# Optimization experiments

Hardware: AMD Instinct MI355X
Metric: run time of the kernel (lower is better)

Reference implementation:

```python
import jax, jax.numpy as jnp
import numpy as np

B, S, D, H = 4, 2048, 1024, 16
HD = D // H
NEG = -1e30


def setup_inputs() -> dict:
    key = jax.random.key(0)
    ks = jax.random.split(key, 6)
    scale = 1.0 / np.sqrt(D)
    return {
        "q": jax.random.normal(ks[0], (B, S, D), jnp.float32),
        "k": jax.random.normal(ks[1], (B, S, D), jnp.float32),
        "v": jax.random.normal(ks[2], (B, S, D), jnp.float32),
        "mask": jnp.ones((B, 1, S), jnp.float32),
        "wq": jax.random.normal(ks[3], (D, D), jnp.float32) * scale,
        "bq": jnp.zeros((D,), jnp.float32),
        "wk": jax.random.normal(ks[4], (D, D), jnp.float32) * scale,
        "bk": jnp.zeros((D,), jnp.float32),
        "wv": jax.random.normal(ks[5], (D, D), jnp.float32) * scale,
        "bv": jnp.zeros((D,), jnp.float32),
    }


def _heads(x):
    # (B,S,D) -> (B,H,S,HD)
    return x.reshape(B, S, H, HD).transpose(0, 2, 1, 3)


def reference(q, k, v, mask, wq, bq, wk, bk, wv, bv):
    # pointwise Conv1D(kernel=1) == linear: x @ W^T + b (W: (out,in))
    qh = _heads(jnp.einsum('bsd,ed->bse', q, wq) + bq)
    kh = _heads(jnp.einsum('bsd,ed->bse', k, wk) + bk)
    vh = _heads(jnp.einsum('bsd,ed->bse', v, wv) + bv)
    scores = jnp.einsum('bhqd,bhkd->bhqk', qh, kh) / jnp.sqrt(jnp.float32(HD))
    # mask_logits: x + (1 - mask) * -1e30, mask (B,1,S) -> (B,1,1,S)
    scores = scores + (1.0 - mask[:, None, :, :]) * NEG
    probs = jax.nn.softmax(scores, axis=-1)  # dropout is identity in eval
    ctx = jnp.einsum('bhqk,bhkd->bhqd', probs, vh)
    return ctx.transpose(0, 2, 1, 3).reshape(B, S, D)
```

## Files before the change

### kernel.cpp

```cpp
#include <hip/hip_runtime.h>
#include <math.h>

typedef __attribute__((ext_vector_type(8)))  _Float16 f16x8;
typedef __attribute__((ext_vector_type(4)))  _Float16 f16x4;
typedef __attribute__((ext_vector_type(2)))  __fp16   h16x2;
typedef __attribute__((ext_vector_type(4)))  float    f32x4;
typedef __attribute__((ext_vector_type(16))) float    f32x16;
typedef unsigned int u32;

static constexpr int B  = 4;
static constexpr int S  = 2048;
static constexpr int D  = 1024;
static constexpr int H  = 16;
static constexpr int HD = 64;

union U64cvt { f16x4 h; ushort4 u; };
union W4 { u32 w[4]; f16x8 v; };

__device__ __forceinline__ void gld16(const void* g, void* l) {
    __builtin_amdgcn_global_load_lds((const u32*)g, (u32*)l, 16, 0, 0);
}

__device__ __forceinline__ void cvtwr16(const float4& x, const float4& y, void* dst) {
    W4 w;
    w.w[0] = __builtin_bit_cast(u32, __builtin_amdgcn_cvt_pkrtz(x.x, x.y));
    w.w[1] = __builtin_bit_cast(u32, __builtin_amdgcn_cvt_pkrtz(x.z, x.w));
    w.w[2] = __builtin_bit_cast(u32, __builtin_amdgcn_cvt_pkrtz(y.x, y.y));
    w.w[3] = __builtin_bit_cast(u32, __builtin_amdgcn_cvt_pkrtz(y.z, y.w));
    *(f16x8*)dst = w.v;
}

__global__ __launch_bounds__(256)
void cvt_prep(const float* __restrict__ q, const float* __restrict__ k,
              const float* __restrict__ v,
              const float* __restrict__ wq, const float* __restrict__ wk,
              const float* __restrict__ wv,
              unsigned short* __restrict__ dst)
{
    const int c = blockIdx.x * 256 + threadIdx.x;
    const float* src;
    size_t idx;
    if (c < 3145728) {
        const int a = c >> 20;
        src = (a == 0) ? q : (a == 1) ? k : v;
        idx = (size_t)(c & 1048575) * 8;
    } else {
        const int c2 = c - 3145728;
        const int a = c2 >> 17;
        src = (a == 0) ? wq : (a == 1) ? wk : wv;
        idx = (size_t)(c2 & 131071) * 8;
    }
    const float4 x = *(const float4*)(src + idx);
    const float4 y = *(const float4*)(src + idx + 4);
    cvtwr16(x, y, dst + (size_t)c * 8);
}

__global__ __launch_bounds__(256)
void proj_f16(const unsigned short* __restrict__ af16,
              const unsigned short* __restrict__ wf16,
              const float* __restrict__ bqp, const float* __restrict__ bkp,
              const float* __restrict__ bvp,
              unsigned short* __restrict__ outs)
{
    const int bid = blockIdx.x;
    const int xcd = bid & 7;
    const int idx = bid >> 3;
    const int z   = idx / 64;
    const int r2  = idx - z * 64;
    const int mpl = r2 >> 3;
    const int np  = r2 & 7;
    const int mp  = (xcd >> 1) * 16 + (xcd & 1) * 8 + mpl;
    const int m0  = mp * 128;
    const int n0  = np * 128;

    const unsigned short* A  = af16 + (size_t)z * 8388608;
    const unsigned short* Wf = wf16 + (size_t)z * 1048576;
    const float* bias = (z == 0) ? bqp : (z == 1) ? bkp : bvp;
    unsigned short* out = outs + (size_t)z * 8388608;

    const int tid  = threadIdx.x;
    const int lane = tid & 63;
    const int wid  = tid >> 6;
    const int wr   = wid >> 1;
    const int wc   = wid & 1;

    __shared__ __align__(16) unsigned char lA[2][8192];
    __shared__ __align__(16) unsigned char lB[2][8192];

    f32x4 acc[4][4];
#pragma unroll
    for (int i = 0; i < 4; ++i)
#pragma unroll
        for (int j = 0; j < 4; ++j) acc[i][j] = (f32x4){0.f, 0.f, 0.f, 0.f};

    int grow[2], gcol[2], lbase[2];
#pragma unroll
    for (int i = 0; i < 2; ++i) {
        const int c = tid + 256 * i;
        grow[i]  = c >> 2;
        gcol[i]  = ((c & 3) - (grow[i] >> 1)) & 3;
        lbase[i] = (c & ~63) * 16;
    }

#pragma unroll
    for (int i = 0; i < 2; ++i) {
        gld16(A  + (size_t)(m0 + grow[i]) * D + gcol[i] * 8, lA[0] + lbase[i]);
        gld16(Wf + (size_t)(n0 + grow[i]) * D + gcol[i] * 8, lB[0] + lbase[i]);
    }
    __syncthreads();

    for (int kt = 0; kt < 32; ++kt) {
        const int cb = kt & 1, nx = cb ^ 1;

        if (kt < 31) {
            const int k1 = (kt + 1) * 32;
#pragma unroll
            for (int i = 0; i < 2; ++i) {
                gld16(A  + (size_t)(m0 + grow[i]) * D + k1 + gcol[i] * 8, lA[nx] + lbase[i]);
                gld16(Wf + (size_t)(n0 + grow[i]) * D + k1 + gcol[i] * 8, lB[nx] + lbase[i]);
            }
        }

        f16x8 af[4], bf[4];
#pragma unroll
        for (int mi = 0; mi < 4; ++mi) {
            const int row = wr * 64 + mi * 16 + (lane & 15);
            const int cc  = ((lane >> 4) + (row >> 1)) & 3;
            af[mi] = *(const f16x8*)(lA[cb] + row * 64 + cc * 16);
        }
#pragma unroll
        for (int ni = 0; ni < 4; ++ni) {
            const int row = wc * 64 + ni * 16 + (lane & 15);
            const int cc  = ((lane >> 4) + (row >> 1)) & 3;
            bf[ni] = *(const f16x8*)(lB[cb] + row * 64 + cc * 16);
        }

        __builtin_amdgcn_s_setprio(1);
#pragma unroll
        for (int mi = 0; mi < 4; ++mi)
#pragma unroll
            for (int ni = 0; ni < 4; ++ni)
                acc[mi][ni] = __builtin_amdgcn_mfma_f32_16x16x32_f16(af[mi], bf[ni], acc[mi][ni], 0, 0, 0);
        __builtin_amdgcn_s_setprio(0);

        __syncthreads();
    }

#pragma unroll
    for (int mi = 0; mi < 4; ++mi) {
        const int gmBase = m0 + wr * 64 + mi * 16 + ((lane >> 4) << 2);
        const int b  = gmBase >> 11;
        const int s0 = gmBase & 2047;
        const int tV   = s0 >> 6;
        const int kv6  = s0 & 63;
        const int ksg  = kv6 >> 4;
        const int hi2v = (kv6 >> 3) & 1;
        const int jb   = kv6 & 7;
#pragma unroll
        for (int ni = 0; ni < 4; ++ni) {
            const int gn = n0 + wc * 64 + ni * 16 + (lane & 15);
            const float bb = bias[gn];
            const int hh = gn >> 6;
            const int hd = gn & 63;
            const size_t bhbase = ((size_t)b * H + hh) * ((size_t)S * HD);
            if (z == 0) {
#pragma unroll
                for (int r = 0; r < 4; ++r) {
                    const int gm = gmBase + r;
                    const _Float16 hv = (_Float16)(acc[mi][ni][r] + bb);
                    out[bhbase + (size_t)(gm & 2047) * HD + hd] =
                        __builtin_bit_cast(unsigned short, hv);
                }
            } else if (z == 1) {
                const int ks   = hd >> 4;
                const int hi2k = (hd >> 3) & 1;
                const int j    = hd & 7;
#pragma unroll
                for (int r = 0; r < 4; ++r) {
                    const int s = (gmBase + r) & 2047;
                    const int t = s >> 6;
                    const int q = ((s >> 5) & 1) * 4 + ks;
                    const _Float16 hv = (_Float16)(acc[mi][ni][r] + bb);
                    out[bhbase + (((size_t)t * 8 + q) * 64 + hi2k * 32 + (s & 31)) * 8 + j] =
                        __builtin_bit_cast(unsigned short, hv);
                }
            } else {
                const int nb  = hd >> 5;
                const int c31 = hd & 31;
                const int q   = nb * 4 + ksg;
                U64cvt uu;
#pragma unroll
                for (int r = 0; r < 4; ++r)
                    uu.h[r] = (_Float16)(acc[mi][ni][r] + bb);
                *(ushort4*)(out + bhbase +
                    (((size_t)tV * 8 + q) * 64 + hi2v * 32 + c31) * 8 + jb) = uu.u;
            }
        }
    }
}

__global__ __launch_bounds__(256)
void proj_qkv(const float* __restrict__ qi, const float* __restrict__ ki,
              const float* __restrict__ vi,
              const float* __restrict__ wqp, const float* __restrict__ wkp,
              const float* __restrict__ wvp,
              const float* __restrict__ bqp, const float* __restrict__ bkp,
              const float* __restrict__ bvp,
              unsigned short* __restrict__ ws)
{
    const int bid = blockIdx.x;
    const int xcd = bid & 7;
    const int idx = bid >> 3;
    const int z   = idx / 64;
    const int r2  = idx - z * 64;
    const int mpl = r2 >> 3;
    const int np  = r2 & 7;
    const int mp  = (xcd >> 1) * 16 + (xcd & 1) * 8 + mpl;
    const int m0  = mp * 128;
    const int n0  = np * 128;

    const float* A    = (z == 0) ? qi  : (z == 1) ? ki  : vi;
    const float* W    = (z == 0) ? wqp : (z == 1) ? wkp : wvp;
    const float* bias = (z == 0) ? bqp : (z == 1) ? bkp : bvp;
    unsigned short* out = ws + (size_t)z * ((size_t)B * S * D);

    const int tid  = threadIdx.x;
    const int lane = tid & 63;
    const int wid  = tid >> 6;
    const int wr   = wid >> 1;
    const int wc   = wid & 1;

    __shared__ __align__(16) unsigned char lA[2][8192];
    __shared__ __align__(16) unsigned char lB[2][8192];

    f32x4 acc[4][4];
#pragma unroll
    for (int i = 0; i < 4; ++i)
#pragma unroll
        for (int j = 0; j < 4; ++j) acc[i][j] = (f32x4){0.f, 0.f, 0.f, 0.f};

    const int rb = (lane >> 4) * 16;

    int srow[2], sc8[2], soff[2];
#pragma unroll
    for (int i = 0; i < 2; ++i) {
        const int f = tid + 256 * i;
        srow[i] = f >> 2;
        sc8[i]  = f & 3;
        soff[i] = ((f >> 2) * 64 + (f & 3) * 16) ^ ((((f >> 2)) & 7) << 4);
    }

#pragma unroll
    for (int i = 0; i < 2; ++i) {
        const float* pa = A + (size_t)(m0 + srow[i]) * D + sc8[i] * 8;
        const float* pw = W + (size_t)(n0 + srow[i]) * D + sc8[i] * 8;
        cvtwr16(*(const float4*)pa, *(const float4*)(pa + 4), lA[0] + soff[i]);
        cvtwr16(*(const float4*)pw, *(const float4*)(pw + 4), lB[0] + soff[i]);
    }
    float4 pa0[2], pa1[2], pw0[2], pw1[2];
#pragma unroll
    for (int i = 0; i < 2; ++i) {
        const float* pa = A + (size_t)(m0 + srow[i]) * D + 32 + sc8[i] * 8;
        const float* pw = W + (size_t)(n0 + srow[i]) * D + 32 + sc8[i] * 8;
        pa0[i] = *(const float4*)pa;  pa1[i] = *(const float4*)(pa + 4);
        pw0[i] = *(const float4*)pw;  pw1[i] = *(const float4*)(pw + 4);
    }
    __syncthreads();

    for (int kt = 0; kt < 32; ++kt) {
        const int cb = kt & 1, nx = cb ^ 1;
        if (kt < 31) {
#pragma unroll
            for (int i = 0; i < 2; ++i) {
                cvtwr16(pa0[i], pa1[i], lA[nx] + soff[i]);
                cvtwr16(pw0[i], pw1[i], lB[nx] + soff[i]);
            }
        }
        f16x8 af[4], bf[4];
#pragma unroll
        for (int mi = 0; mi < 4; ++mi) {
            const int row = wr * 64 + mi * 16 + (lane & 15);
            af[mi] = *(const f16x8*)(lA[cb] + ((row * 64 + rb) ^ ((row & 7) << 4)));
        }
#pragma unroll
        for (int ni = 0; ni < 4; ++ni) {
            const int row = wc * 64 + ni * 16 + (lane & 15);
            bf[ni] = *(const f16x8*)(lB[cb] + ((row * 64 + rb) ^ ((row & 7) << 4)));
        }
        if (kt < 30) {
            const int k2 = (kt + 2) * 32;
#pragma unroll
            for (int i = 0; i < 2; ++i) {
                const float* pa = A + (size_t)(m0 + srow[i]) * D + k2 + sc8[i] * 8;
                const float* pw = W + (size_t)(n0 + srow[i]) * D + k2 + sc8[i] * 8;
                pa0[i] = *(const float4*)pa;  pa1[i] = *(const float4*)(pa + 4);
                pw0[i] = *(const float4*)pw;  pw1[i] = *(const float4*)(pw + 4);
            }
        }
        __builtin_amdgcn_s_setprio(1);
#pragma unroll
        for (int mi = 0; mi < 4; ++mi)
#pragma unroll
            for (int ni = 0; ni < 4; ++ni)
                acc[mi][ni] = __builtin_amdgcn_mfma_f32_16x16x32_f16(af[mi], bf[ni], acc[mi][ni], 0, 0, 0);
        __builtin_amdgcn_s_setprio(0);
        __syncthreads();
    }

#pragma unroll
    for (int mi = 0; mi < 4; ++mi) {
        const int gmBase = m0 + wr * 64 + mi * 16 + ((lane >> 4) << 2);
        const int b  = gmBase >> 11;
        const int s0 = gmBase & 2047;
        const int tV   = s0 >> 6;
        const int kv6  = s0 & 63;
        const int ksg  = kv6 >> 4;
        const int hi2v = (kv6 >> 3) & 1;
        const int jb   = kv6 & 7;
#pragma unroll
        for (int ni = 0; ni < 4; ++ni) {
            const int gn = n0 + wc * 64 + ni * 16 + (lane & 15);
            const float bb = bias[gn];
            const int hh = gn >> 6;
            const int hd = gn & 63;
            const size_t bhbase = ((size_t)b * H + hh) * ((size_t)S * HD);
            if (z == 0) {
#pragma unroll
                for (int r = 0; r < 4; ++r) {
                    const int gm = gmBase + r;
                    const _Float16 hv = (_Float16)(acc[mi][ni][r] + bb);
                    out[bhbase + (size_t)(gm & 2047) * HD + hd] =
                        __builtin_bit_cast(unsigned short, hv);
                }
            } else if (z == 1) {
                const int ks   = hd >> 4;
                const int hi2k = (hd >> 3) & 1;
                const int j    = hd & 7;
#pragma unroll
                for (int r = 0; r < 4; ++r) {
                    const int s = (gmBase + r) & 2047;
                    const int t = s >> 6;
                    const int q = ((s >> 5) & 1) * 4 + ks;
                    const _Float16 hv = (_Float16)(acc[mi][ni][r] + bb);
                    out[bhbase + (((size_t)t * 8 + q) * 64 + hi2k * 32 + (s & 31)) * 8 + j] =
                        __builtin_bit_cast(unsigned short, hv);
                }
            } else {
                const int nb  = hd >> 5;
                const int c31 = hd & 31;
                const int q   = nb * 4 + ksg;
                U64cvt uu;
#pragma unroll
                for (int r = 0; r < 4; ++r)
                    uu.h[r] = (_Float16)(acc[mi][ni][r] + bb);
                *(ushort4*)(out + bhbase +
                    (((size_t)tV * 8 + q) * 64 + hi2v * 32 + c31) * 8 + jb) = uu.u;
            }
        }
    }
}

__global__ __launch_bounds__(256)
void attn_f16(const unsigned short* __restrict__ qh,
              const unsigned short* __restrict__ kf,
              const unsigned short* __restrict__ vf,
              const float* __restrict__ mask,
              float* __restrict__ out)
{
    const int flat = blockIdx.y * gridDim.x + blockIdx.x;
    const int sw   = (flat & 7) * 128 + (flat >> 3);
    const int bh   = sw >> 4;
    const int q0   = (sw & 15) * 128;

    const int b = bh >> 4;
    const int h = bh & 15;
    const unsigned short* Q  = qh + (size_t)bh * S * HD;
    const unsigned short* KF = kf + (size_t)bh * S * HD;
    const unsigned short* VF = vf + (size_t)bh * S * HD;

    const int tid  = threadIdx.x;
    const int lane = tid & 63;
    const int wid  = tid >> 6;
    const int l31  = lane & 31;
    const int hi2  = lane >> 5;

    __shared__ __align__(16) unsigned char Kl[2][8192];
    __shared__ __align__(16) unsigned char Vl[2][8192];
    __shared__ __align__(16) float maskb[2][64];

    const int ldsA = wid * 1024;
    const int ldsB = wid * 1024 + 4096;
    const int g0   = tid * 8;
    const int g1   = tid * 8 + 2048;

    const float C = 0.18033688011112042f;
    const float SHIFT = -5.770780163555854f;

    f16x8 aq[4];
    {
        const unsigned short* qrow = Q + (size_t)(q0 + wid * 32 + l31) * HD;
#pragma unroll
        for (int ks = 0; ks < 4; ++ks)
            aq[ks] = *(const f16x8*)(qrow + ks * 16 + hi2 * 8);
    }

    float ls0 = 0.f, ls1 = 0.f;
    f32x16 accO[2];
    accO[0] = (f32x16){};
    accO[1] = (f32x16){};
    const h16x2 one2 = {(__fp16)1.0f, (__fp16)1.0f};

    gld16(KF + g0, Kl[0] + ldsA);
    gld16(KF + g1, Kl[0] + ldsB);
    gld16(VF + g0, Vl[0] + ldsA);
    gld16(VF + g1, Vl[0] + ldsB);
    if (tid < 64)
        maskb[0][tid] = fmaf(1.0f - mask[(size_t)b * S + tid], -1.4426950408889634e30f, SHIFT);
    __syncthreads();

    const int lane16 = lane * 16;
    for (int t = 0; t < S / 64; ++t) {
        const int cb = t & 1, nx = cb ^ 1;
        const unsigned char* Kc = Kl[cb];
        const unsigned char* Vc = Vl[cb];

        if (t < S / 64 - 1) {
            const int nt = (t + 1) * 4096;
            gld16(KF + nt + g0, Kl[nx] + ldsA);
            gld16(KF + nt + g1, Kl[nx] + ldsB);
            gld16(VF + nt + g0, Vl[nx] + ldsA);
            gld16(VF + nt + g1, Vl[nx] + ldsB);
            if (tid < 64)
                maskb[nx][tid] = fmaf(1.0f - mask[(size_t)b * S + (t + 1) * 64 + tid],
                                      -1.4426950408889634e30f, SHIFT);
        }

        f32x16 p[2];
        p[0] = (f32x16){};
        p[1] = (f32x16){};
        __builtin_amdgcn_s_setprio(1);
#pragma unroll
        for (int kb = 0; kb < 2; ++kb)
#pragma unroll
            for (int ks = 0; ks < 4; ++ks) {
                const f16x8 ak = *(const f16x8*)(Kc + lane16 + (kb * 4 + ks) * 1024);
                p[kb] = __builtin_amdgcn_mfma_f32_32x32x16_f16(ak, aq[ks], p[kb], 0, 0, 0);
            }
        __builtin_amdgcn_s_setprio(0);

        f16x8 pa[4];
#pragma unroll
        for (int kb = 0; kb < 2; ++kb) {
            float pe[16];
#pragma unroll
            for (int g = 0; g < 4; ++g) {
                const f32x4 mg = *(const f32x4*)(&maskb[cb][kb * 32 + g * 8 + hi2 * 4]);
#pragma unroll
                for (int e = 0; e < 4; ++e)
                    pe[g * 4 + e] = exp2f(fmaf(p[kb][g * 4 + e], C, mg[e]));
            }
#pragma unroll
            for (int ks2 = 0; ks2 < 2; ++ks2) {
                const int o = ks2 * 8;
                const h16x2 h0 = __builtin_amdgcn_cvt_pkrtz(pe[o + 0], pe[o + 1]);
                const h16x2 h1 = __builtin_amdgcn_cvt_pkrtz(pe[o + 2], pe[o + 3]);
                const h16x2 h2 = __builtin_amdgcn_cvt_pkrtz(pe[o + 4], pe[o + 5]);
                const h16x2 h3 = __builtin_amdgcn_cvt_pkrtz(pe[o + 6], pe[o + 7]);
                ls0 = __builtin_amdgcn_fdot2(h0, one2, ls0, false);
                ls1 = __builtin_amdgcn_fdot2(h1, one2, ls1, false);
                ls0 = __builtin_amdgcn_fdot2(h2, one2, ls0, false);
                ls1 = __builtin_amdgcn_fdot2(h3, one2, ls1, false);
                u32 a0 = __builtin_bit_cast(u32, h0);
                u32 a1 = __builtin_bit_cast(u32, h1);
                u32 a2 = __builtin_bit_cast(u32, h2);
                u32 a3 = __builtin_bit_cast(u32, h3);
                asm volatile("v_permlane32_swap_b32 %0, %1" : "+v"(a0), "+v"(a2));
                asm volatile("v_permlane32_swap_b32 %0, %1" : "+v"(a1), "+v"(a3));
                W4 w;
                w.w[0] = a0; w.w[1] = a1; w.w[2] = a2; w.w[3] = a3;
                pa[kb * 2 + ks2] = w.v;
            }
        }

        __builtin_amdgcn_s_setprio(1);
#pragma unroll
        for (int nb = 0; nb < 2; ++nb)
#pragma unroll
            for (int ksg = 0; ksg < 4; ++ksg) {
                const f16x8 bv = *(const f16x8*)(Vc + lane16 + (nb * 4 + ksg) * 1024);
                accO[nb] = __builtin_amdgcn_mfma_f32_32x32x16_f16(pa[ksg], bv, accO[nb], 0, 0, 0);
            }
        __builtin_amdgcn_s_setprio(0);

        __syncthreads();
    }

    float lsum = ls0 + ls1;
    lsum += __shfl_xor(lsum, 32);
    const float linv = 1.0f / lsum;

    float lr[16];
#pragma unroll
    for (int r = 0; r < 16; ++r)
        lr[r] = __shfl(linv, (r & 3) + 8 * (r >> 2) + 4 * hi2);

#pragma unroll
    for (int nb = 0; nb < 2; ++nb) {
        const int dcol = h * HD + nb * 32 + l31;
#pragma unroll
        for (int r = 0; r < 16; ++r) {
            const int qrow = q0 + wid * 32 + (r & 3) + 8 * (r >> 2) + 4 * hi2;
            out[((size_t)b * S + qrow) * D + dcol] = accO[nb][r] * lr[r];
        }
    }
}

extern "C" void kernel_launch(void* const* d_in, const int* in_sizes, int n_in,
                              void* d_out, int out_size, void* d_ws, size_t ws_size,
                              hipStream_t stream)
{
    const float* q    = (const float*)d_in[0];
    const float* k    = (const float*)d_in[1];
    const float* v    = (const float*)d_in[2];
    const float* mask = (const float*)d_in[3];
    const float* wq   = (const float*)d_in[4];
    const float* bq   = (const float*)d_in[5];
    const float* wk   = (const float*)d_in[6];
    const float* bk   = (const float*)d_in[7];
    const float* wv   = (const float*)d_in[8];
    const float* bv   = (const float*)d_in[9];

    unsigned short* ws = (unsigned short*)d_ws;
    const size_t per  = (size_t)B * S * D;
    const size_t wsz  = 1048576;
    const size_t need = (3 * per + 3 * wsz + 3 * per) * 2;

    dim3 ga(S / 128, B * H);
    if (ws_size >= need) {
        unsigned short* af16 = ws;
        unsigned short* wf16 = ws + 3 * per;
        unsigned short* outs = ws + 3 * per + 3 * wsz;
        cvt_prep<<<13824, 256, 0, stream>>>(q, k, v, wq, wk, wv, af16);
        proj_f16<<<1536, 256, 0, stream>>>(af16, wf16, bq, bk, bv, outs);
        attn_f16<<<ga, 256, 0, stream>>>(outs, outs + per, outs + 2 * per, mask, (float*)d_out);
    } else {
        proj_qkv<<<1536, 256, 0, stream>>>(q, k, v, wq, wk, wv, bq, bk, bv, ws);
        attn_f16<<<ga, 256, 0, stream>>>(ws, ws + per, ws + 2 * per, mask, (float*)d_out);
    }
}
```

Before: 224.7 us.

## Fold softmax scale into Q projection and mask bias into extra MFMA

```diff
diff --git a/kernel.cpp b/kernel.cpp
--- a/kernel.cpp
+++ b/kernel.cpp
@@ -13,6 +13,9 @@
 static constexpr int D  = 1024;
 static constexpr int H  = 16;
 static constexpr int HD = 64;
+
+#define CSCALE 0.18033688011112042f
+#define MSHIFT -5.770780163555854f
 
 union U64cvt { f16x4 h; ushort4 u; };
 union W4 { u32 w[4]; f16x8 v; };
@@ -56,6 +59,23 @@
 }
 
 __global__ __launch_bounds__(256)
+void mf_prep(const float* __restrict__ mask, unsigned short* __restrict__ mf)
+{
+    const int cm   = blockIdx.x * 256 + threadIdx.x;
+    const int b    = cm >> 12;
+    const int rem  = cm & 4095;
+    const int t    = rem >> 7;
+    const int kb   = (rem >> 6) & 1;
+    const int lane = rem & 63;
+    const int kv   = t * 64 + kb * 32 + (lane & 31);
+    const float m  = fmaf(1.0f - mask[(size_t)b * S + kv], -30000.0f, MSHIFT);
+    W4 w;
+    w.w[0] = __builtin_bit_cast(u32, __builtin_amdgcn_cvt_pkrtz(m, 0.0f));
+    w.w[1] = 0; w.w[2] = 0; w.w[3] = 0;
+    *(f16x8*)(mf + (size_t)cm * 8) = w.v;
+}
+
+__global__ __launch_bounds__(256)
 void proj_f16(const unsigned short* __restrict__ af16,
               const unsigned short* __restrict__ wf16,
               const float* __restrict__ bqp, const float* __restrict__ bkp,
@@ -167,7 +187,7 @@
 #pragma unroll
                 for (int r = 0; r < 4; ++r) {
                     const int gm = gmBase + r;
-                    const _Float16 hv = (_Float16)(acc[mi][ni][r] + bb);
+                    const _Float16 hv = (_Float16)((acc[mi][ni][r] + bb) * CSCALE);
                     out[bhbase + (size_t)(gm & 2047) * HD + hd] =
                         __builtin_bit_cast(unsigned short, hv);
                 }
@@ -328,7 +348,7 @@
 #pragma unroll
                 for (int r = 0; r < 4; ++r) {
                     const int gm = gmBase + r;
-                    const _Float16 hv = (_Float16)(acc[mi][ni][r] + bb);
+                    const _Float16 hv = (_Float16)((acc[mi][ni][r] + bb) * CSCALE);
                     out[bhbase + (size_t)(gm & 2047) * HD + hd] =
                         __builtin_bit_cast(unsigned short, hv);
                 }
@@ -364,7 +384,7 @@
 void attn_f16(const unsigned short* __restrict__ qh,
               const unsigned short* __restrict__ kf,
               const unsigned short* __restrict__ vf,
-              const float* __restrict__ mask,
+              const unsigned short* __restrict__ mf,
               float* __restrict__ out)
 {
     const int flat = blockIdx.y * gridDim.x + blockIdx.x;
@@ -377,6 +397,7 @@
     const unsigned short* Q  = qh + (size_t)bh * S * HD;
     const unsigned short* KF = kf + (size_t)bh * S * HD;
     const unsigned short* VF = vf + (size_t)bh * S * HD;
+    const unsigned short* MFb = mf + (size_t)b * 32768;
 
     const int tid  = threadIdx.x;
     const int lane = tid & 63;
@@ -386,16 +407,12 @@
 
     __shared__ __align__(16) unsigned char Kl[2][8192];
     __shared__ __align__(16) unsigned char Vl[2][8192];
-    __shared__ __align__(16) float maskb[2][64];
 
     const int ldsA = wid * 1024;
     const int ldsB = wid * 1024 + 4096;
     const int g0   = tid * 8;
     const int g1   = tid * 8 + 2048;
 
-    const float C = 0.18033688011112042f;
-    const float SHIFT = -5.770780163555854f;
-
     f16x8 aq[4];
     {
         const unsigned short* qrow = Q + (size_t)(q0 + wid * 32 + l31) * HD;
@@ -403,6 +420,11 @@
         for (int ks = 0; ks < 4; ++ks)
             aq[ks] = *(const f16x8*)(qrow + ks * 16 + hi2 * 8);
     }
+
+    f16x8 aqone = {};
+    if (hi2 == 0) aqone[0] = (_Float16)1.0f;
+
+    f32x16 fzero = {};
 
     float ls0 = 0.f, ls1 = 0.f;
     f32x16 accO[2];
@@ -414,8 +436,8 @@
     gld16(KF + g1, Kl[0] + ldsB);
     gld16(VF + g0, Vl[0] + ldsA);
     gld16(VF + g1, Vl[0] + ldsB);
-    if (tid < 64)
-        maskb[0][tid] = fmaf(1.0f - mask[(size_t)b * S + tid], -1.4426950408889634e30f, SHIFT);
+    f16x8 mfc0 = *(const f16x8*)(MFb + lane * 8);
+    f16x8 mfc1 = *(const f16x8*)(MFb + 512 + lane * 8);
     __syncthreads();
 
     const int lane16 = lane * 16;
@@ -424,28 +446,32 @@
         const unsigned char* Kc = Kl[cb];
         const unsigned char* Vc = Vl[cb];
 
+        f16x8 mfn0, mfn1;
         if (t < S / 64 - 1) {
             const int nt = (t + 1) * 4096;
             gld16(KF + nt + g0, Kl[nx] + ldsA);
             gld16(KF + nt + g1, Kl[nx] + ldsB);
             gld16(VF + nt + g0, Vl[nx] + ldsA);
             gld16(VF + nt + g1, Vl[nx] + ldsB);
-            if (tid < 64)
-                maskb[nx][tid] = fmaf(1.0f - mask[(size_t)b * S + (t + 1) * 64 + tid],
-                                      -1.4426950408889634e30f, SHIFT);
+            mfn0 = *(const f16x8*)(MFb + (t + 1) * 1024 + lane * 8);
+            mfn1 = *(const f16x8*)(MFb + (t + 1) * 1024 + 512 + lane * 8);
         }
 
         f32x16 p[2];
-        p[0] = (f32x16){};
-        p[1] = (f32x16){};
         __builtin_amdgcn_s_setprio(1);
 #pragma unroll
-        for (int kb = 0; kb < 2; ++kb)
-#pragma unroll
-            for (int ks = 0; ks < 4; ++ks) {
+        for (int kb = 0; kb < 2; ++kb) {
+            {
+                const f16x8 ak = *(const f16x8*)(Kc + lane16 + (kb * 4 + 0) * 1024);
+                p[kb] = __builtin_amdgcn_mfma_f32_32x32x16_f16(ak, aq[0], fzero, 0, 0, 0);
+            }
+#pragma unroll
+            for (int ks = 1; ks < 4; ++ks) {
                 const f16x8 ak = *(const f16x8*)(Kc + lane16 + (kb * 4 + ks) * 1024);
                 p[kb] = __builtin_amdgcn_mfma_f32_32x32x16_f16(ak, aq[ks], p[kb], 0, 0, 0);
             }
+            p[kb] = __builtin_amdgcn_mfma_f32_32x32x16_f16(kb == 0 ? mfc0 : mfc1, aqone, p[kb], 0, 0, 0);
+        }
         __builtin_amdgcn_s_setprio(0);
 
         f16x8 pa[4];
@@ -453,12 +479,8 @@
         for (int kb = 0; kb < 2; ++kb) {
             float pe[16];
 #pragma unroll
-            for (int g = 0; g < 4; ++g) {
-                const f32x4 mg = *(const f32x4*)(&maskb[cb][kb * 32 + g * 8 + hi2 * 4]);
-#pragma unroll
-                for (int e = 0; e < 4; ++e)
-                    pe[g * 4 + e] = exp2f(fmaf(p[kb][g * 4 + e], C, mg[e]));
-            }
+            for (int e = 0; e < 16; ++e)
+                pe[e] = exp2f(p[kb][e]);
 #pragma unroll
             for (int ks2 = 0; ks2 < 2; ++ks2) {
                 const int o = ks2 * 8;
@@ -492,6 +514,8 @@
             }
         __builtin_amdgcn_s_setprio(0);
 
+        mfc0 = mfn0;
+        mfc1 = mfn1;
         __syncthreads();
     }
 
@@ -533,18 +557,23 @@
     unsigned short* ws = (unsigned short*)d_ws;
     const size_t per  = (size_t)B * S * D;
     const size_t wsz  = 1048576;
-    const size_t need = (3 * per + 3 * wsz + 3 * per) * 2;
+    const size_t mfsz = 131072;
+    const size_t need = (3 * per + 3 * wsz + 3 * per + mfsz) * 2;
 
     dim3 ga(S / 128, B * H);
     if (ws_size >= need) {
         unsigned short* af16 = ws;
         unsigned short* wf16 = ws + 3 * per;
         unsigned short* outs = ws + 3 * per + 3 * wsz;
+        unsigned short* mfp  = outs + 3 * per;
+        mf_prep<<<64, 256, 0, stream>>>(mask, mfp);
         cvt_prep<<<13824, 256, 0, stream>>>(q, k, v, wq, wk, wv, af16);
         proj_f16<<<1536, 256, 0, stream>>>(af16, wf16, bq, bk, bv, outs);
-        attn_f16<<<ga, 256, 0, stream>>>(outs, outs + per, outs + 2 * per, mask, (float*)d_out);
+        attn_f16<<<ga, 256, 0, stream>>>(outs, outs + per, outs + 2 * per, mfp, (float*)d_out);
     } else {
+        unsigned short* mfp = ws + 3 * per;
+        mf_prep<<<64, 256, 0, stream>>>(mask, mfp);
         proj_qkv<<<1536, 256, 0, stream>>>(q, k, v, wq, wk, wv, bq, bk, bv, ws);
-        attn_f16<<<ga, 256, 0, stream>>>(ws, ws + per, ws + 2 * per, mask, (float*)d_out);
-    }
-}
+        attn_f16<<<ga, 256, 0, stream>>>(ws, ws + per, ws + 2 * per, mfp, (float*)d_out);
+    }
+}
```

Result: slower. 230.0 us (+2.4%).
